# Performance work log

Measured on AMD Instinct MI355X. Metric: run time of the kernel, lower is better.

## Reference

```python
import jax, jax.numpy as jnp
import numpy as np

# Fixed problem geometry: B equal-sized graphs with contiguous node ids.
B, N, E, F_IN, H, C = 64, 1024, 655360, 128, 128, 10
K1 = int(np.ceil(0.8 * N))    # 820 nodes/graph kept by pool1
K2 = int(np.ceil(0.8 * K1))   # 656 nodes/graph kept by pool2


def setup_inputs() -> dict:
    key = jax.random.key(0)
    ks = jax.random.split(key, 12)
    x = jax.random.normal(ks[0], (B * N, F_IN), jnp.float32)
    # intra-graph random edges, E//B per graph
    e_per = E // B
    local = jax.random.randint(ks[1], (2, E), 0, N)
    off = jnp.repeat(jnp.arange(B, dtype=jnp.int32) * N, e_per)
    edge_index = (local + off[None, :]).astype(jnp.int32)
    batch = jnp.repeat(jnp.arange(B, dtype=jnp.int32), N)

    def lin(k, i, o):
        return jax.random.normal(k, (i, o), jnp.float32) / np.sqrt(i)

    return {
        "x": x, "edge_index": edge_index, "batch": batch,
        "Wl1": lin(ks[2], F_IN, H), "bl1": jnp.zeros((H,), jnp.float32), "Wr1": lin(ks[3], F_IN, H),
        "Wl2": lin(ks[4], H, H),    "bl2": jnp.zeros((H,), jnp.float32), "Wr2": lin(ks[5], H, H),
        "pw1": jax.random.normal(ks[6], (H,), jnp.float32) / np.sqrt(H),
        "pw2": jax.random.normal(ks[7], (H,), jnp.float32) / np.sqrt(H),
        "fW1": lin(ks[8], 2 * H, H), "fb1": jnp.zeros((H,), jnp.float32),
        "fW2": lin(ks[9], H, C),     "fb2": jnp.zeros((C,), jnp.float32),
    }


def _sage(x, src, dst, em, Wl, bl, Wr, n):
    # PyG SAGEConv (aggr='mean'): lin_l(mean_{j->i} x_j) + lin_r(x_i)
    msg = x[src] * em[:, None]                                   # [E, d]
    s = jax.ops.segment_sum(msg, dst, num_segments=n)            # [n, d]
    cnt = jax.ops.segment_sum(em, dst, num_segments=n)           # [n]
    mean = s / jnp.maximum(cnt, 1.0)[:, None]
    return mean @ Wl + bl + x @ Wr


def _topk_pool(x, src, dst, em, n_per, k, w):
    # PyG TopKPooling: score = tanh(x.w/||w||); keep top-k per graph; gate kept x by score.
    score = jnp.tanh(x @ w / jnp.linalg.norm(w))                 # [B*n_per]
    _, idx = jax.lax.top_k(score.reshape(B, n_per), k)           # [B, k]
    idx = jnp.sort(idx, axis=1)
    perm = (idx + (jnp.arange(B) * n_per)[:, None]).reshape(-1)  # global kept ids [B*k]
    nx = x[perm] * score[perm][:, None]
    # relabel edges; drop edges touching removed nodes via mask
    inv = jnp.full((B * n_per,), -1, jnp.int32).at[perm].set(jnp.arange(B * k, dtype=jnp.int32))
    ns, nd = inv[src], inv[dst]
    nm = em * (ns >= 0).astype(x.dtype) * (nd >= 0).astype(x.dtype)
    return nx, jnp.maximum(ns, 0), jnp.maximum(nd, 0), nm


def _readout(h, k):
    g = h.reshape(B, k, H)
    return jnp.concatenate([g.mean(axis=1), g.max(axis=1)], axis=1)  # [B, 2H]


def reference(x, edge_index, batch, Wl1, bl1, Wr1, Wl2, bl2, Wr2,
              pw1, pw2, fW1, fb1, fW2, fb2):
    src, dst = edge_index[0], edge_index[1]
    em = jnp.ones((E,), x.dtype)
    h = jax.nn.relu(_sage(x, src, dst, em, Wl1, bl1, Wr1, B * N))
    h, src, dst, em = _topk_pool(h, src, dst, em, N, K1, pw1)
    x1 = _readout(h, K1)
    h = jax.nn.relu(_sage(h, src, dst, em, Wl2, bl2, Wr2, B * K1))
    h, src, dst, em = _topk_pool(h, src, dst, em, K1, K2, pw2)
    x2 = _readout(h, K2)
    z = jax.nn.relu((x1 + x2) @ fW1 + fb1)
    # dropout is identity in eval mode
    return z @ fW2 + fb2
```

## Files before the change

### kernel.cpp

```cpp
#include <hip/hip_runtime.h>
#include <cstdint>
#include <cstddef>

namespace {

constexpr int kB    = 64;
constexpr int kN    = 1024;
constexpr int kE    = 655360;
constexpr int kEper = kE / kB;
constexpr int kH    = 128;
constexpr int kK1   = 820;
constexpr int kK2   = 656;
constexpr int kM1   = kB * kN;
constexpr int kM2   = kB * kK1;

typedef __attribute__((ext_vector_type(8))) short bf16x8;
typedef __attribute__((ext_vector_type(4))) float f32x4;

__device__ inline ushort f2bf(float f) {
  uint u = __float_as_uint(f);
  return (ushort)((u + 0x7fffu + ((u >> 16) & 1u)) >> 16);
}
__device__ inline float bf2f(ushort s) { return __uint_as_float(((uint)s) << 16); }

__device__ inline void cvt4(const float* f, uint* hh, uint* ll) {
#pragma unroll
  for (int i = 0; i < 2; ++i) {
    uint h;
    asm("v_cvt_pk_bf16_f32 %0, %1, %2" : "=v"(h) : "v"(f[2 * i]), "v"(f[2 * i + 1]));
    const float r0 = __uint_as_float(h << 16);
    const float r1 = __uint_as_float(h & 0xFFFF0000u);
    const float d0 = f[2 * i] - r0;
    const float d1 = f[2 * i + 1] - r1;
    uint l;
    asm("v_cvt_pk_bf16_f32 %0, %1, %2" : "=v"(l) : "v"(d0), "v"(d1));
    hh[i] = h; ll[i] = l;
  }
}

__device__ inline void llds16(const void* g, void* l) {
  __builtin_amdgcn_global_load_lds(
      (const __attribute__((address_space(1))) void*)g,
      (__attribute__((address_space(3))) void*)l, 16, 0, 0);
}

__device__ inline int block_scan_1024(int v, int* wsum ) {
  const int lane = threadIdx.x & 63;
  const int w    = threadIdx.x >> 6;
#pragma unroll
  for (int off = 1; off < 64; off <<= 1) {
    const int n = __shfl_up(v, off);
    if (lane >= off) v += n;
  }
  if (lane == 63) wsum[w] = v;
  __syncthreads();
  if (w == 0) {
    int s = (lane < 16) ? wsum[lane] : 0;
#pragma unroll
    for (int off = 1; off < 16; off <<= 1) {
      const int n = __shfl_up(s, off);
      if (lane >= off) s += n;
    }
    if (lane < 16) wsum[lane] = s;
  }
  __syncthreads();
  if (w > 0) v += wsum[w - 1];
  return v;
}

__device__ inline void radix_select(uint key, int K, int* hist, uint* bTp,
                                    int* bRemp, uint& T, int& rem_out) {
  const int tid = threadIdx.x;
  uint prefix = 0;
  int rem = K;
#pragma unroll
  for (int shift = 24; shift >= 0; shift -= 8) {
    if (tid < 256) hist[tid] = 0;
    __syncthreads();
    const uint mask = (shift == 24) ? 0u : (0xFFFFFFFFu << (shift + 8));
    if ((key & mask) == prefix)
      atomicAdd(&hist[(key >> shift) & 255], 1);
    __syncthreads();
    if (tid < 64) {
      const int h0 = hist[4 * tid + 0], h1 = hist[4 * tid + 1];
      const int h2 = hist[4 * tid + 2], h3 = hist[4 * tid + 3];
      const int loc = h0 + h1 + h2 + h3;
      int suf = loc;
#pragma unroll
      for (int d = 1; d < 64; d <<= 1) {
        const int o = __shfl_down(suf, d);
        if (tid + d < 64) suf += o;
      }
      const int above = suf - loc;
      int hs[5];
      hs[4] = above;
      hs[3] = above + h3;
      hs[2] = hs[3] + h2;
      hs[1] = hs[2] + h1;
      hs[0] = hs[1] + h0;
#pragma unroll
      for (int q = 0; q < 4; ++q) {
        if (hs[q] >= rem && hs[q + 1] < rem) {
          *bTp   = prefix | ((uint)(4 * tid + q) << shift);
          *bRemp = rem - hs[q + 1];
        }
      }
    }
    __syncthreads();
    prefix = *bTp;
    rem    = *bRemp;
    __syncthreads();
  }
  T = prefix;
  rem_out = rem;
}

__device__ inline uint score_key(float sc) {
  const uint bits = __float_as_uint(sc);
  return (bits & 0x80000000u) ? ~bits : (bits | 0x80000000u);
}

__global__ __launch_bounds__(1024)
void build_prep(const int* __restrict__ src, const int* __restrict__ dst,
                int* __restrict__ coff, int* __restrict__ ccur,
                int* __restrict__ ent,
                const float* __restrict__ Wl1, const float* __restrict__ Wr1,
                const float* __restrict__ Wl2, const float* __restrict__ Wr2,
                const float* __restrict__ pw1, const float* __restrict__ pw2,
                ushort* __restrict__ W1h, ushort* __restrict__ W1l,
                ushort* __restrict__ W2h, ushort* __restrict__ W2l,
                float* __restrict__ pwn1, float* __restrict__ pwn2) {
  const int b   = blockIdx.x;
  const int tid = threadIdx.x;
  if (b >= 128) {
    if (tid >= 256) return;
    const float* pw = (tid < 128) ? pw1 : pw2;
    float* o        = (tid < 128) ? pwn1 : pwn2;
    const int j = tid & 127;
    float sum = 0.0f;
    for (int k = 0; k < 128; ++k) { const float v = pw[k]; sum += v * v; }
    o[j] = pw[j] / sqrtf(sum);
    return;
  }
  if (b >= 64) {
    const int ob  = (b - 64) * 4 + (tid >> 8);
    const bool l2 = ob >= 128;
    const int idx = (ob & 127) * 256 + (tid & 255);
    const int n = idx >> 8, k = idx & 255;
    const float* Wl = l2 ? Wl2 : Wl1;
    const float* Wr = l2 ? Wr2 : Wr1;
    const float w = (k < 128) ? Wl[k * kH + n] : Wr[(k - 128) * kH + n];
    const ushort h = f2bf(w);
    (l2 ? W2h : W1h)[n * 256 + k] = h;
    (l2 ? W2l : W1l)[n * 256 + k] = f2bf(w - bf2f(h));
    return;
  }
  __shared__ int cnt[1024];
  __shared__ int wsum[16];
  const int g = ((b & 7) << 3) + (b >> 3);
  const int ebase = g * kEper;
  cnt[tid] = 0;
  __syncthreads();
  for (int e = tid; e < kEper; e += 1024)
    atomicAdd(&cnt[dst[ebase + e] & (kN - 1)], 1);
  __syncthreads();
  const int dg   = cnt[tid];
  const int incl = block_scan_1024(dg, wsum);
  const int start = ebase + incl - dg;
  coff[g * kN + tid] = start;
  ccur[g * kN + tid] = start + dg;
  __syncthreads();
  cnt[tid] = start;
  __syncthreads();
  for (int e = tid; e < kEper; e += 1024) {
    const int d   = dst[ebase + e] & (kN - 1);
    const int pos = atomicAdd(&cnt[d], 1);
    ent[pos] = src[ebase + e] & (kN - 1);
  }
}

__global__ __launch_bounds__(1024, 8)
void gather1_lds(const float* __restrict__ feat, const int* __restrict__ ent,
                 const int* __restrict__ off, const int* __restrict__ cursor,
                 float* __restrict__ aggout) {
  __shared__ float cache[1024 * 16];
  const int xcd   = blockIdx.x & 7;
  const int local = blockIdx.x >> 3;
  const int graph = xcd * 8 + (local >> 3);
  const int chunk = local & 7;
  const int tid   = threadIdx.x;
  const int wid   = tid >> 6;
  const int gbase = graph << 10;

#pragma unroll
  for (int ps = 0; ps < 4; ++ps) {
    const int row = ps * 256 + (tid >> 2);
    const int q   = (tid & 3) * 4;
    llds16(feat + (size_t)(gbase + row) * kH + chunk * 16 + q,
           cache + ps * 4096 + wid * 256);
  }
  __syncthreads();

  const int grp = tid >> 2;
  const int q4  = (tid & 3) * 4;

  for (int it = 0; it < 4; ++it) {
    const int lnode = it * 256 + grp;
    const int node  = gbase + lnode;
    const int o0 = off[node];
    const int o1 = cursor[node];
    const int deg = o1 - o0;
    float4 acc = make_float4(0.f, 0.f, 0.f, 0.f);
    int pf[4];
#pragma unroll
    for (int i = 0; i < 4; ++i) pf[i] = (o0 + i < o1) ? ent[o0 + i] : 0;
    for (int eb = 0; eb < deg; eb += 4) {
      int nx[4];
#pragma unroll
      for (int i = 0; i < 4; ++i) {
        const int idx = o0 + eb + 4 + i;
        nx[i] = (idx < o1) ? ent[idx] : 0;
      }
#pragma unroll
      for (int i = 0; i < 4; ++i) {
        const float m = (eb + i < deg) ? 1.0f : 0.0f;
        const float4 v = *(const float4*)&cache[pf[i] * 16 + q4];
        acc.x = fmaf(v.x, m, acc.x);
        acc.y = fmaf(v.y, m, acc.y);
        acc.z = fmaf(v.z, m, acc.z);
        acc.w = fmaf(v.w, m, acc.w);
      }
#pragma unroll
      for (int i = 0; i < 4; ++i) pf[i] = nx[i];
    }
    const float r = 1.0f / fmaxf((float)deg, 1.0f);
    const f32x4 res = {acc.x * r, acc.y * r, acc.z * r, acc.w * r};
    *(f32x4*)(aggout + (size_t)node * kH + chunk * 16 + q4) = res;
  }
}

__global__ __launch_bounds__(1024, 8)
void gather2_lds(const float* __restrict__ feat, const int* __restrict__ ent,
                 const int* __restrict__ off, const int* __restrict__ cursor,
                 const int* __restrict__ perm, const float* __restrict__ gsg,
                 float* __restrict__ aggout,
                 float* __restrict__ psumg, float* __restrict__ pmaxg) {
  __shared__ float cache[1024 * 16];
  __shared__ float gs[1024];
  __shared__ float rps[16][16], rpm[16][16];
  const int xcd   = blockIdx.x & 7;
  const int local = blockIdx.x >> 3;
  const int graph = xcd * 8 + (local >> 3);
  const int chunk = local & 7;
  const int tid   = threadIdx.x;
  const int wid   = tid >> 6;
  const int gbase = graph << 10;

#pragma unroll
  for (int ps = 0; ps < 4; ++ps) {
    const int row = ps * 256 + (tid >> 2);
    const int q   = (tid & 3) * 4;
    llds16(feat + (size_t)(gbase + row) * kH + chunk * 16 + q,
           cache + ps * 4096 + wid * 256);
  }
  gs[tid] = gsg[gbase + tid];
  __syncthreads();

  const int grp = tid >> 2;
  const int q4  = (tid & 3) * 4;

  for (int it = 0; it < 4; ++it) {
    const int lnode = it * 256 + grp;
    int o0 = 0, o1 = 0;
    if (lnode < kK1) {
      const int orig = perm[graph * kK1 + lnode];
      o0 = off[orig];
      o1 = cursor[orig];
    }
    const int deg = o1 - o0;
    float4 acc = make_float4(0.f, 0.f, 0.f, 0.f);
    int cnt = 0;
    int pf[4];
#pragma unroll
    for (int i = 0; i < 4; ++i) pf[i] = (o0 + i < o1) ? ent[o0 + i] : 0;
    for (int eb = 0; eb < deg; eb += 4) {
      int nx[4];
#pragma unroll
      for (int i = 0; i < 4; ++i) {
        const int idx = o0 + eb + 4 + i;
        nx[i] = (idx < o1) ? ent[idx] : 0;
      }
#pragma unroll
      for (int i = 0; i < 4; ++i) {
        const float raw  = gs[pf[i]];
        const bool  kept = (raw > 0.5f) && (eb + i < deg);
        const float s    = kept ? raw - 2.0f : 0.0f;
        cnt += kept ? 1 : 0;
        const float4 v = *(const float4*)&cache[pf[i] * 16 + q4];
        acc.x = fmaf(v.x, s, acc.x);
        acc.y = fmaf(v.y, s, acc.y);
        acc.z = fmaf(v.z, s, acc.z);
        acc.w = fmaf(v.w, s, acc.w);
      }
#pragma unroll
      for (int i = 0; i < 4; ++i) pf[i] = nx[i];
    }
    const float r = 1.0f / fmaxf((float)cnt, 1.0f);
    const f32x4 res = {acc.x * r, acc.y * r, acc.z * r, acc.w * r};
    if (lnode < kK1)
      *(f32x4*)(aggout + (size_t)(graph * kK1 + lnode) * kH + chunk * 16 + q4) = res;
  }

  __syncthreads();
  const int rcol = tid & 15;
  const int rseg = tid >> 4;
  float rs = 0.0f, rm = -1e30f;
#pragma unroll
  for (int i = 0; i < 16; ++i) {
    const int row = rseg * 16 + i;
    const float raw = gs[row];
    if (raw > 0.5f) {
      const float v = cache[row * 16 + rcol] * (raw - 2.0f);
      rs += v;
      rm = fmaxf(rm, v);
    }
  }
  rs += __shfl_xor(rs, 16); rs += __shfl_xor(rs, 32);
  rm = fmaxf(rm, __shfl_xor(rm, 16)); rm = fmaxf(rm, __shfl_xor(rm, 32));
  if ((tid & 48) == 0) { rps[wid][rcol] = rs; rpm[wid][rcol] = rm; }
  __syncthreads();
  if (tid < 16) {
    float ts = 0.0f, tm = -1e30f;
#pragma unroll
    for (int w = 0; w < 16; ++w) { ts += rps[w][tid]; tm = fmaxf(tm, rpm[w][tid]); }
    psumg[graph * kH + chunk * 16 + tid] = ts;
    pmaxg[graph * kH + chunk * 16 + tid] = tm;
  }
}

__global__ __launch_bounds__(256)
void sage_gemm_mfma(const float* __restrict__ meanb, const float* __restrict__ xsrc,
                    const int* __restrict__ perm, const float* __restrict__ gsc,
                    const ushort* __restrict__ WTh, const ushort* __restrict__ WTl,
                    const float* __restrict__ bias, const float* __restrict__ pwn,
                    float* __restrict__ outp, float* __restrict__ scr,
                    int cpx, int nblk) {
  __shared__ __align__(16) ushort aH[64][32];
  __shared__ __align__(16) ushort aL[64][32];
  __shared__ __align__(16) ushort wHs[128][32];
  __shared__ __align__(16) ushort wLs[128][32];
  __shared__ float sdot[64][2];
  const int vb = (blockIdx.x & 7) * cpx + (blockIdx.x >> 3);
  if (vb >= nblk) return;
  const int tid  = threadIdx.x;
  const int wid  = tid >> 6;
  const int lane = tid & 63;
  const int quad = lane >> 4;
  const int l16  = lane & 15;
  const int rowbase = vb * 64;
  const int wr = (wid >> 1) * 32;
  const int wc = (wid & 1) * 64;

  const int n0a = wid * 32;
  const int n0b = wid * 32 + 16;
  const int wrowa = (n0a + (lane >> 2)) * 256 + (lane & 3) * 8;
  const int wrowb = (n0b + (lane >> 2)) * 256 + (lane & 3) * 8;

  int srow1[2]; float scl1[2];
#pragma unroll
  for (int i = 0; i < 2; ++i) {
    const int grow = rowbase + ((tid + i * 256) >> 3);
    srow1[i] = grow; scl1[i] = 1.0f;
    if (perm) { srow1[i] = perm[grow]; scl1[i] = gsc[grow]; }
  }

  f32x4 acc[2][4];
#pragma unroll
  for (int a = 0; a < 2; ++a)
#pragma unroll
    for (int b = 0; b < 4; ++b) acc[a][b] = (f32x4){0.f, 0.f, 0.f, 0.f};

  for (int s = 0; s < 8; ++s) {
    const bool ismean = s < 4;
    const float* sp = ismean ? meanb : xsrc;
    const int kbase = s * 32;
    const int kloc  = ismean ? kbase : kbase - 128;
#pragma unroll
    for (int i = 0; i < 2; ++i) {
      const int p   = tid + i * 256;
      const int row = p >> 3;
      const int k4  = (p & 7) * 4;
      const int srow   = ismean ? (rowbase + row) : srow1[i];
      const float scale = ismean ? 1.0f : scl1[i];
      const float4 v = *(const float4*)(sp + (size_t)srow * kH + kloc + k4);
      float f[4] = {v.x * scale, v.y * scale, v.z * scale, v.w * scale};
      uint hh[2], ll[2];
      cvt4(f, hh, ll);
      *(uint2*)&aH[row][k4] = make_uint2(hh[0], hh[1]);
      *(uint2*)&aL[row][k4] = make_uint2(ll[0], ll[1]);
    }
    llds16(WTh + wrowa + kbase, &wHs[n0a][0]);
    llds16(WTh + wrowb + kbase, &wHs[n0b][0]);
    llds16(WTl + wrowa + kbase, &wLs[n0a][0]);
    llds16(WTl + wrowb + kbase, &wLs[n0b][0]);
    __syncthreads();
    bf16x8 afh[2], afl[2];
#pragma unroll
    for (int rt = 0; rt < 2; ++rt) {
      afh[rt] = *(const bf16x8*)&aH[wr + rt * 16 + l16][quad * 8];
      afl[rt] = *(const bf16x8*)&aL[wr + rt * 16 + l16][quad * 8];
    }
#pragma unroll
    for (int ct = 0; ct < 4; ++ct) {
      const bf16x8 bh = *(const bf16x8*)&wHs[wc + ct * 16 + l16][quad * 8];
      const bf16x8 bl = *(const bf16x8*)&wLs[wc + ct * 16 + l16][quad * 8];
#pragma unroll
      for (int rt = 0; rt < 2; ++rt) {
        acc[rt][ct] = __builtin_amdgcn_mfma_f32_16x16x32_bf16(afh[rt], bh, acc[rt][ct], 0, 0, 0);
        acc[rt][ct] = __builtin_amdgcn_mfma_f32_16x16x32_bf16(afh[rt], bl, acc[rt][ct], 0, 0, 0);
        acc[rt][ct] = __builtin_amdgcn_mfma_f32_16x16x32_bf16(afl[rt], bh, acc[rt][ct], 0, 0, 0);
      }
    }
    __syncthreads();
  }
  float bv[4], pwv[4];
#pragma unroll
  for (int ct = 0; ct < 4; ++ct) {
    const int col = wc + ct * 16 + l16;
    bv[ct]  = bias[col];
    pwv[ct] = pwn[col];
  }
  float dot[2][4];
#pragma unroll
  for (int rt = 0; rt < 2; ++rt)
#pragma unroll
    for (int reg = 0; reg < 4; ++reg) dot[rt][reg] = 0.0f;
#pragma unroll
  for (int ct = 0; ct < 4; ++ct) {
    const int col = wc + ct * 16 + l16;
#pragma unroll
    for (int rt = 0; rt < 2; ++rt) {
#pragma unroll
      for (int reg = 0; reg < 4; ++reg) {
        const int row = rowbase + wr + rt * 16 + quad * 4 + reg;
        const float o = fmaxf(acc[rt][ct][reg] + bv[ct], 0.0f);
        outp[(size_t)row * kH + col] = o;
        dot[rt][reg] += o * pwv[ct];
      }
    }
  }
#pragma unroll
  for (int rt = 0; rt < 2; ++rt) {
#pragma unroll
    for (int reg = 0; reg < 4; ++reg) {
      float d = dot[rt][reg];
      d += __shfl_xor(d, 1);
      d += __shfl_xor(d, 2);
      d += __shfl_xor(d, 4);
      d += __shfl_xor(d, 8);
      if (l16 == 0) sdot[wr + rt * 16 + quad * 4 + reg][wc >> 6] = d;
    }
  }
  __syncthreads();
  if (tid < 64) scr[rowbase + tid] = tanhf(sdot[tid][0] + sdot[tid][1]);
}

__global__ __launch_bounds__(1024)
void rank_compact(const float* __restrict__ scr, int n_per, int K,
                  int* __restrict__ perm, float* __restrict__ gsc,
                  float* __restrict__ gsg) {
  __shared__ int hist[256];
  __shared__ int wsum[16];
  __shared__ uint bT;
  __shared__ int bRem;
  const int g = ((blockIdx.x & 7) << 3) + (blockIdx.x >> 3);
  const int tid = threadIdx.x;
  const float sc = (tid < n_per) ? scr[g * n_per + tid] : -3e30f;
  const uint key = score_key(sc);

  uint T; int rem;
  radix_select(key, K, hist, &bT, &bRem, T, rem);

  const int gt = (key > T) ? 1 : 0;
  const int eq = (key == T) ? 1 : 0;
  const int incl = block_scan_1024((gt << 11) | eq, wsum);
  const int excl = incl - ((gt << 11) | eq);
  const int gt_excl = excl >> 11;
  const int eq_excl = excl & 2047;
  const int keep = (tid < n_per) && (gt || (eq && eq_excl < rem));
  if (keep) {
    const int pos = gt_excl + min(eq_excl, rem);
    perm[g * K + pos] = g * n_per + tid;
    gsc[g * K + pos]  = sc;
  }
  if (gsg) gsg[g * kN + tid] = keep ? sc + 2.0f : 0.0f;
}

__global__ __launch_bounds__(1024)
void final_fused(const float* __restrict__ scr, const float* __restrict__ h2,
                 const float* __restrict__ ps1, const float* __restrict__ pm1,
                 const float* __restrict__ fW1, const float* __restrict__ fb1,
                 const float* __restrict__ fW2, const float* __restrict__ fb2,
                 float* __restrict__ out) {
  __shared__ int hist[256];
  __shared__ int wsum[16];
  __shared__ uint bT;
  __shared__ int bRem;
  __shared__ float ls[1024];
  __shared__ float ss[8][128], sm[8][128];
  __shared__ float xx[256];
  __shared__ float z[128];
  const int g = ((blockIdx.x & 7) << 3) + (blockIdx.x >> 3);
  const int tid = threadIdx.x;
  const int n_per = kK1, K = kK2;

  const float sc = (tid < n_per) ? scr[g * n_per + tid] : -3e30f;
  const uint key = score_key(sc);
  uint T; int rem;
  radix_select(key, K, hist, &bT, &bRem, T, rem);
  const int gt = (key > T) ? 1 : 0;
  const int eq = (key == T) ? 1 : 0;
  const int eq_incl = block_scan_1024(eq, wsum);
  const int eq_excl = eq_incl - eq;
  const int keep = (tid < n_per) && (gt || (eq && eq_excl < rem));
  ls[tid] = keep ? sc + 2.0f : 0.0f;
  __syncthreads();

  const int part = tid >> 7;
  const int j    = tid & 127;
  const float* h2g = h2 + (size_t)g * kK1 * kH + j;
  float sum = 0.0f, mx = -1e30f;
  for (int i = part; i < n_per; i += 32) {
    float v[4], s[4];
#pragma unroll
    for (int u = 0; u < 4; ++u) {
      const int ii = i + u * 8;
      const bool ok = ii < n_per;
      s[u] = ok ? ls[ii] : 0.0f;
      v[u] = ok ? h2g[(size_t)ii * kH] : 0.0f;
    }
#pragma unroll
    for (int u = 0; u < 4; ++u) {
      const float val = v[u] * (s[u] - 2.0f);
      if (s[u] > 0.5f) { sum += val; mx = fmaxf(mx, val); }
    }
  }
  ss[part][j] = sum;
  sm[part][j] = mx;
  __syncthreads();

  if (tid < 128) {
    float s2 = 0.0f, m2 = -1e30f;
#pragma unroll
    for (int p = 0; p < 8; ++p) { s2 += ss[p][tid]; m2 = fmaxf(m2, sm[p][tid]); }
    const float s1 = ps1[(size_t)g * 128 + tid];
    const float m1 = pm1[(size_t)g * 128 + tid];
    xx[tid]       = s1 / (float)kK1 + s2 / (float)K;
    xx[tid + 128] = m1 + m2;
  }
  __syncthreads();
  if (tid < 128) {
    float a = fb1[tid];
    for (int k = 0; k < 256; ++k) a += xx[k] * fW1[k * 128 + tid];
    z[tid] = fmaxf(a, 0.0f);
  }
  __syncthreads();
  if (tid < 10) {
    float o = fb2[tid];
    for (int k = 0; k < 128; ++k) o += z[k] * fW2[k * 10 + tid];
    out[g * 10 + tid] = o;
  }
}

}

extern "C" void kernel_launch(void* const* d_in, const int* in_sizes, int n_in,
                              void* d_out, int out_size, void* d_ws, size_t ws_size,
                              hipStream_t stream) {
  const float* x   = (const float*)d_in[0];
  const int*   ei  = (const int*)d_in[1];
  const float* Wl1 = (const float*)d_in[3];
  const float* bl1 = (const float*)d_in[4];
  const float* Wr1 = (const float*)d_in[5];
  const float* Wl2 = (const float*)d_in[6];
  const float* bl2 = (const float*)d_in[7];
  const float* Wr2 = (const float*)d_in[8];
  const float* pw1 = (const float*)d_in[9];
  const float* pw2 = (const float*)d_in[10];
  const float* fW1 = (const float*)d_in[11];
  const float* fb1 = (const float*)d_in[12];
  const float* fW2 = (const float*)d_in[13];
  const float* fb2 = (const float*)d_in[14];
  const int* src = ei;
  const int* dst = ei + kE;
  (void)in_sizes; (void)n_in; (void)out_size; (void)ws_size;

  char* wsb = (char*)d_ws;
  size_t off_b = 0;
  auto alloc = [&](size_t bytes) {
    void* p = wsb + off_b;
    off_b += (bytes + 255) & ~(size_t)255;
    return p;
  };
  float* bufA = (float*)alloc((size_t)kM1 * kH * 4);
  float* bufB = (float*)alloc((size_t)kM1 * kH * 4);
  float* bufC = (float*)alloc((size_t)kM2 * kH * 4);
  int*   coff = (int*)alloc((size_t)kM1 * 4);
  int*   ccur = (int*)alloc((size_t)kM1 * 4);
  int*   ent  = (int*)alloc((size_t)kE * 4);
  float* scr  = (float*)alloc((size_t)kM1 * 4);
  float* gsg  = (float*)alloc((size_t)kM1 * 4);
  int*   perm1= (int*)alloc((size_t)kM2 * 4);
  float* gsc1 = (float*)alloc((size_t)kM2 * 4);
  float* psum1= (float*)alloc((size_t)kB * 128 * 4);
  float* pmax1= (float*)alloc((size_t)kB * 128 * 4);
  ushort* wt1h = (ushort*)alloc((size_t)128 * 256 * 2);
  ushort* wt1l = (ushort*)alloc((size_t)128 * 256 * 2);
  ushort* wt2h = (ushort*)alloc((size_t)128 * 256 * 2);
  ushort* wt2l = (ushort*)alloc((size_t)128 * 256 * 2);
  float* pwn1 = (float*)alloc(128 * 4);
  float* pwn2 = (float*)alloc(128 * 4);

  build_prep<<<129, 1024, 0, stream>>>(src, dst, coff, ccur, ent,
                                       Wl1, Wr1, Wl2, Wr2, pw1, pw2,
                                       wt1h, wt1l, wt2h, wt2l, pwn1, pwn2);

  gather1_lds<<<kB * 8, 1024, 0, stream>>>(x, ent, coff, ccur, bufA);
  sage_gemm_mfma<<<kM1 / 64, 256, 0, stream>>>(bufA, x, nullptr, nullptr,
                                               wt1h, wt1l, bl1, pwn1, bufB, scr,
                                               128, kM1 / 64);
  rank_compact<<<kB, 1024, 0, stream>>>(scr, kN, kK1, perm1, gsc1, gsg);

  gather2_lds<<<kB * 8, 1024, 0, stream>>>(bufB, ent, coff, ccur, perm1, gsg,
                                           bufA, psum1, pmax1);
  sage_gemm_mfma<<<824, 256, 0, stream>>>(bufA, bufB, perm1, gsc1,
                                          wt2h, wt2l, bl2, pwn2, bufC, scr,
                                          103, kM2 / 64);
  final_fused<<<kB, 1024, 0, stream>>>(scr, bufC, psum1, pmax1,
                                       fW1, fb1, fW2, fb2, (float*)d_out);
}
```

Baseline: 239.1 us.

## Fuse pool1 top-k rank/compact into layer-1 GEMM via last-block-per-graph counter

Removes the separate rank_compact launch. Each GEMM block now bumps a per-graph atomic counter, and the 16th block to finish a graph runs the radix select and compaction over that graph's 1024 scores. It uses 256 threads, each handling 4 nodes, and reuses GEMM shared memory for the histogram. This saves one kernel launch and lets ranking overlap with the remaining GEMM blocks, at the cost of threadfence/atomic overhead and a serialized tail in the last block of each graph.

```diff
diff --git a/kernel.cpp b/kernel.cpp
--- a/kernel.cpp
+++ b/kernel.cpp
@@ -123,7 +123,7 @@
 __global__ __launch_bounds__(1024)
 void build_prep(const int* __restrict__ src, const int* __restrict__ dst,
                 int* __restrict__ coff, int* __restrict__ ccur,
-                int* __restrict__ ent,
+                int* __restrict__ ent, int* __restrict__ gcnt,
                 const float* __restrict__ Wl1, const float* __restrict__ Wr1,
                 const float* __restrict__ Wl2, const float* __restrict__ Wr2,
                 const float* __restrict__ pw1, const float* __restrict__ pw2,
@@ -133,6 +133,7 @@
   const int b   = blockIdx.x;
   const int tid = threadIdx.x;
   if (b >= 128) {
+    if (tid < 64) gcnt[tid] = 0;
     if (tid >= 256) return;
     const float* pw = (tid < 128) ? pw1 : pw2;
     float* o        = (tid < 128) ? pwn1 : pwn2;
@@ -344,12 +345,18 @@
                     const ushort* __restrict__ WTh, const ushort* __restrict__ WTl,
                     const float* __restrict__ bias, const float* __restrict__ pwn,
                     float* __restrict__ outp, float* __restrict__ scr,
-                    int cpx, int nblk) {
+                    int cpx, int nblk, int rankK, int* __restrict__ gcnt,
+                    int* __restrict__ rperm, float* __restrict__ rgsc,
+                    float* __restrict__ rgsg) {
   __shared__ __align__(16) ushort aH[64][32];
   __shared__ __align__(16) ushort aL[64][32];
   __shared__ __align__(16) ushort wHs[128][32];
   __shared__ __align__(16) ushort wLs[128][32];
   __shared__ float sdot[64][2];
+  __shared__ int lastFlag;
+  __shared__ uint rbT;
+  __shared__ int rbRem;
+  __shared__ int wsum4[4];
   const int vb = (blockIdx.x & 7) * cpx + (blockIdx.x >> 3);
   if (vb >= nblk) return;
   const int tid  = threadIdx.x;
@@ -463,37 +470,102 @@
   }
   __syncthreads();
   if (tid < 64) scr[rowbase + tid] = tanhf(sdot[tid][0] + sdot[tid][1]);
-}
-
-__global__ __launch_bounds__(1024)
-void rank_compact(const float* __restrict__ scr, int n_per, int K,
-                  int* __restrict__ perm, float* __restrict__ gsc,
-                  float* __restrict__ gsg) {
-  __shared__ int hist[256];
-  __shared__ int wsum[16];
-  __shared__ uint bT;
-  __shared__ int bRem;
-  const int g = ((blockIdx.x & 7) << 3) + (blockIdx.x >> 3);
-  const int tid = threadIdx.x;
-  const float sc = (tid < n_per) ? scr[g * n_per + tid] : -3e30f;
-  const uint key = score_key(sc);
-
-  uint T; int rem;
-  radix_select(key, K, hist, &bT, &bRem, T, rem);
-
-  const int gt = (key > T) ? 1 : 0;
-  const int eq = (key == T) ? 1 : 0;
-  const int incl = block_scan_1024((gt << 11) | eq, wsum);
-  const int excl = incl - ((gt << 11) | eq);
-  const int gt_excl = excl >> 11;
-  const int eq_excl = excl & 2047;
-  const int keep = (tid < n_per) && (gt || (eq && eq_excl < rem));
-  if (keep) {
-    const int pos = gt_excl + min(eq_excl, rem);
-    perm[g * K + pos] = g * n_per + tid;
-    gsc[g * K + pos]  = sc;
-  }
-  if (gsg) gsg[g * kN + tid] = keep ? sc + 2.0f : 0.0f;
+
+  if (rankK) {
+    __threadfence();
+    __syncthreads();
+    const int gg = vb >> 4;
+    if (tid == 0) lastFlag = (atomicAdd(&gcnt[gg], 1) == 15);
+    __syncthreads();
+    if (lastFlag) {
+      __threadfence();
+      int* hist = (int*)&aL[0][0];
+      float sc4[4]; uint key4[4];
+#pragma unroll
+      for (int i = 0; i < 4; ++i) {
+        sc4[i]  = scr[gg * kN + tid * 4 + i];
+        key4[i] = score_key(sc4[i]);
+      }
+      uint prefix = 0; int rem = rankK;
+#pragma unroll
+      for (int shift = 24; shift >= 0; shift -= 8) {
+        hist[tid] = 0;
+        __syncthreads();
+        const uint mask = (shift == 24) ? 0u : (0xFFFFFFFFu << (shift + 8));
+#pragma unroll
+        for (int i = 0; i < 4; ++i)
+          if ((key4[i] & mask) == prefix)
+            atomicAdd(&hist[(key4[i] >> shift) & 255], 1);
+        __syncthreads();
+        if (tid < 64) {
+          const int h0 = hist[4 * tid + 0], h1 = hist[4 * tid + 1];
+          const int h2 = hist[4 * tid + 2], h3 = hist[4 * tid + 3];
+          const int loc = h0 + h1 + h2 + h3;
+          int suf = loc;
+#pragma unroll
+          for (int d = 1; d < 64; d <<= 1) {
+            const int o = __shfl_down(suf, d);
+            if (tid + d < 64) suf += o;
+          }
+          const int above = suf - loc;
+          int hs[5];
+          hs[4] = above;
+          hs[3] = above + h3;
+          hs[2] = hs[3] + h2;
+          hs[1] = hs[2] + h1;
+          hs[0] = hs[1] + h0;
+#pragma unroll
+          for (int q = 0; q < 4; ++q) {
+            if (hs[q] >= rem && hs[q + 1] < rem) {
+              rbT   = prefix | ((uint)(4 * tid + q) << shift);
+              rbRem = rem - hs[q + 1];
+            }
+          }
+        }
+        __syncthreads();
+        prefix = rbT;
+        rem    = rbRem;
+        __syncthreads();
+      }
+      int run = 0, loc4[4], gt4[4], eq4[4];
+#pragma unroll
+      for (int i = 0; i < 4; ++i) {
+        gt4[i] = (key4[i] > prefix) ? 1 : 0;
+        eq4[i] = (key4[i] == prefix) ? 1 : 0;
+        loc4[i] = run;
+        run += (gt4[i] << 11) | eq4[i];
+      }
+      int incv = run;
+#pragma unroll
+      for (int off = 1; off < 64; off <<= 1) {
+        const int n = __shfl_up(incv, off);
+        if (lane >= off) incv += n;
+      }
+      if (lane == 63) wsum4[wid] = incv;
+      __syncthreads();
+      if (tid == 0) {
+        int r = 0;
+#pragma unroll
+        for (int i = 0; i < 4; ++i) { const int t = wsum4[i]; wsum4[i] = r; r += t; }
+      }
+      __syncthreads();
+      const int tbase = wsum4[wid] + incv - run;
+#pragma unroll
+      for (int i = 0; i < 4; ++i) {
+        const int node = tid * 4 + i;
+        const int excl = tbase + loc4[i];
+        const int gt_excl = excl >> 11;
+        const int eq_excl = excl & 2047;
+        const int keep = gt4[i] || (eq4[i] && eq_excl < rem);
+        if (keep) {
+          const int pos = gt_excl + min(eq_excl, rem);
+          rperm[gg * rankK + pos] = gg * kN + node;
+          rgsc[gg * rankK + pos]  = sc4[i];
+        }
+        rgsg[gg * kN + node] = keep ? sc4[i] + 2.0f : 0.0f;
+      }
+    }
+  }
 }
 
 __global__ __launch_bounds__(1024)
@@ -614,6 +686,7 @@
   float* gsc1 = (float*)alloc((size_t)kM2 * 4);
   float* psum1= (float*)alloc((size_t)kB * 128 * 4);
   float* pmax1= (float*)alloc((size_t)kB * 128 * 4);
+  int*   gcnt = (int*)alloc((size_t)kB * 4);
   ushort* wt1h = (ushort*)alloc((size_t)128 * 256 * 2);
   ushort* wt1l = (ushort*)alloc((size_t)128 * 256 * 2);
   ushort* wt2h = (ushort*)alloc((size_t)128 * 256 * 2);
@@ -621,21 +694,22 @@
   float* pwn1 = (float*)alloc(128 * 4);
   float* pwn2 = (float*)alloc(128 * 4);
 
-  build_prep<<<129, 1024, 0, stream>>>(src, dst, coff, ccur, ent,
+  build_prep<<<129, 1024, 0, stream>>>(src, dst, coff, ccur, ent, gcnt,
                                        Wl1, Wr1, Wl2, Wr2, pw1, pw2,
                                        wt1h, wt1l, wt2h, wt2l, pwn1, pwn2);
 
   gather1_lds<<<kB * 8, 1024, 0, stream>>>(x, ent, coff, ccur, bufA);
   sage_gemm_mfma<<<kM1 / 64, 256, 0, stream>>>(bufA, x, nullptr, nullptr,
                                                wt1h, wt1l, bl1, pwn1, bufB, scr,
-                                               128, kM1 / 64);
-  rank_compact<<<kB, 1024, 0, stream>>>(scr, kN, kK1, perm1, gsc1, gsg);
+                                               128, kM1 / 64,
+                                               kK1, gcnt, perm1, gsc1, gsg);
 
   gather2_lds<<<kB * 8, 1024, 0, stream>>>(bufB, ent, coff, ccur, perm1, gsg,
                                            bufA, psum1, pmax1);
   sage_gemm_mfma<<<824, 256, 0, stream>>>(bufA, bufB, perm1, gsc1,
                                           wt2h, wt2l, bl2, pwn2, bufC, scr,
-                                          103, kM2 / 64);
+                                          103, kM2 / 64,
+                                          0, nullptr, nullptr, nullptr, nullptr);
   final_fused<<<kB, 1024, 0, stream>>>(scr, bufC, psum1, pmax1,
                                        fW1, fb1, fW2, fb2, (float*)d_out);
 }
```

New measurement: 358.7 us. +50.1%, slower.
